# Performance work log

Measured on AMD Instinct MI355X. Metric: run time of the kernel, lower is better.

## Reference

```python
import jax, jax.numpy as jnp
import numpy as np

# Lloyd-Max (Max 1960) optimal 16-level quantizer for N(0,1), bits=4
_CODEBOOK_4 = np.array([-2.7326, -2.069, -1.6181, -1.2562, -0.9424, -0.6568,
                        -0.3881, -0.1284, 0.1284, 0.3881, 0.6568, 0.9424,
                        1.2562, 1.6181, 2.069, 2.7326], dtype=np.float32)
DIM = 256


def setup_inputs() -> dict:
    key = jax.random.key(0)
    kx, kq = jax.random.split(key)
    x = jax.random.normal(kx, (4, 4096, DIM), dtype=jnp.float32)
    # orthogonal rotation via QR of a Gaussian matrix (mirrors torch.linalg.qr)
    rotation, _ = jnp.linalg.qr(jax.random.normal(kq, (DIM, DIM), dtype=jnp.float32))
    codebook = jnp.asarray(_CODEBOOK_4)
    return {"x": x, "rotation": rotation, "codebook": codebook}


def reference(x, rotation, codebook):
    shape = x.shape
    d = shape[-1]
    sqrt_d = jnp.sqrt(jnp.asarray(d, dtype=x.dtype))
    x_flat = x.reshape(-1, d)                                   # (N, d)
    x_norm = jnp.maximum(
        jnp.linalg.norm(x_flat, axis=-1, keepdims=True), 1e-8)  # (N, 1)
    u = x_flat / x_norm                                         # unit vectors
    y_scaled = (u @ rotation.T) * sqrt_d                        # ~N(0,1) coords
    # nearest codebook entry per scalar coordinate: (N, d, K) -> argmin over K
    idx = jnp.argmin(jnp.abs(y_scaled[..., None] - codebook), axis=-1)
    y_hat = codebook[idx] / sqrt_d                              # (N, d)
    x_hat = (y_hat @ rotation) * x_norm                         # de-rotate, rescale
    return x_hat.reshape(shape)
```

## Files before the change

### kernel.cpp

```cpp
#include <hip/hip_runtime.h>

typedef _Float16 f16;
typedef _Float16 f16x4 __attribute__((ext_vector_type(4)));
typedef _Float16 f16x8 __attribute__((ext_vector_type(8)));
typedef float f32x16 __attribute__((ext_vector_type(16)));
typedef float f32x4 __attribute__((ext_vector_type(4)));

#define APITCH 264
#define WREG 67584

__global__ __launch_bounds__(1024) void prep_kernel(const float* __restrict__ R,
                                                    f16* __restrict__ ws) {
  __shared__ float Lrs[32][260];
  const int g = blockIdx.x;
  const int t = threadIdx.x;
  f16* W1h = ws;
  f16* W1l = ws + WREG;
  f16* W2h = ws + 2 * WREG;

  #pragma unroll
  for (int it = 0; it < 2; ++it) {
    int c = it * 1024 + t;
    int row = c >> 6, c4 = (c & 63) * 4;
    f32x4 v = *(const f32x4*)&R[(long)(32 * g + row) * 256 + c4];
    *(f32x4*)&Lrs[row][c4] = v;
  }
  __syncthreads();

  {
    int f_loc = t >> 6, l = t & 63;
    int k0 = 16 * f_loc + 8 * (l >> 5);
    const float* src = &Lrs[l & 31][k0];
    f16x8 h, lo;
    #pragma unroll
    for (int j = 0; j < 8; ++j) {
      float v = src[j] * 256.0f;
      f16 hh = (f16)v;
      h[j] = hh;
      lo[j] = (f16)(v - (float)hh);
    }
    long o = (long)(g * 16 + f_loc) * 512 + l * 8;
    *(f16x8*)(W1h + o) = h;
    *(f16x8*)(W1l + o) = lo;
  }

  {
    int gp = t >> 7, e = (t >> 6) & 1, l = t & 63;
    int lr0 = 16 * e + 8 * (l >> 5);
    int col = 32 * gp + (l & 31);
    f16x8 h;
    #pragma unroll
    for (int j = 0; j < 8; ++j) h[j] = (f16)Lrs[lr0 + j][col];
    long o = (long)(gp * 16 + 2 * g + e) * 512 + l * 8;
    *(f16x8*)(W2h + o) = h;
  }
}

__global__ __launch_bounds__(512, 4) void tq_main(
    const float* __restrict__ X, const float* __restrict__ CB,
    const f16* __restrict__ ws, float* __restrict__ OUT) {
  __shared__ f16 A1h[32][APITCH];
  __shared__ f16 A1l[32][APITCH];
  __shared__ float s2s[32];

  const int tid = threadIdx.x;
  const int lane = tid & 63;
  const int wv = tid >> 6;
  const int lrow = lane & 31;
  const int kg = lane >> 5;
  const long row0 = (long)blockIdx.x * 32;

  const f16* W1h = ws;
  const f16* W1l = ws + WREG;
  const f16* W2h = ws + 2 * WREG;

  const int r = tid >> 4, q = tid & 15;
  const float* xp = X + (row0 + r) * 256 + q * 16;
  float xa[16];
  #pragma unroll
  for (int i = 0; i < 4; ++i) {
    f32x4 v = ((const f32x4*)xp)[i];
    xa[4 * i] = v.x; xa[4 * i + 1] = v.y; xa[4 * i + 2] = v.z; xa[4 * i + 3] = v.w;
  }
  float ss = 0.f;
  #pragma unroll
  for (int i = 0; i < 16; ++i) ss += xa[i] * xa[i];
  ss += __shfl_xor(ss, 8, 16);
  ss += __shfl_xor(ss, 4, 16);
  ss += __shfl_xor(ss, 2, 16);
  ss += __shfl_xor(ss, 1, 16);
  float nrm = fmaxf(sqrtf(ss), 1e-8f);
  float s1f = 4096.0f / nrm;
  if (q == 0) s2s[r] = nrm * 0.0625f;

  #pragma unroll
  for (int c8 = 0; c8 < 2; ++c8) {
    f16x8 h, l;
    #pragma unroll
    for (int j = 0; j < 8; ++j) {
      float a = xa[c8 * 8 + j] * s1f;
      f16 hh = (f16)a;
      h[j] = hh;
      l[j] = (f16)(a - (float)hh);
    }
    *(f16x8*)&A1h[r][q * 16 + c8 * 8] = h;
    *(f16x8*)&A1l[r][q * 16 + c8 * 8] = l;
  }
  __syncthreads();

  const f16* W1hp = W1h + (long)(wv * 16) * 512 + lane * 8;
  const f16* W1lp = W1l + (long)(wv * 16) * 512 + lane * 8;
  f16x8 bh0 = *(const f16x8*)(W1hp);
  f16x8 bl0 = *(const f16x8*)(W1lp);
  f16x8 bh1 = *(const f16x8*)(W1hp + 512);
  f16x8 bl1 = *(const f16x8*)(W1lp + 512);

  f32x16 zv;
  #pragma unroll
  for (int i = 0; i < 16; ++i) zv[i] = 0.0f;
  f32x16 accH = zv, accL = zv;

  #pragma unroll
  for (int ks = 0; ks < 16; ks += 2) {
    {
      const int k0 = ks * 16 + kg * 8;
      f16x8 ah = *(const f16x8*)&A1h[lrow][k0];
      f16x8 al = *(const f16x8*)&A1l[lrow][k0];
      accH = __builtin_amdgcn_mfma_f32_32x32x16_f16(ah, bh0, accH, 0, 0, 0);
      accL = __builtin_amdgcn_mfma_f32_32x32x16_f16(al, bh0, accL, 0, 0, 0);
      accH = __builtin_amdgcn_mfma_f32_32x32x16_f16(ah, bl0, accH, 0, 0, 0);
      accL = __builtin_amdgcn_mfma_f32_32x32x16_f16(al, bl0, accL, 0, 0, 0);
      bh0 = *(const f16x8*)(W1hp + (ks + 2) * 512);
      bl0 = *(const f16x8*)(W1lp + (ks + 2) * 512);
    }
    {
      const int k0 = (ks + 1) * 16 + kg * 8;
      f16x8 ah = *(const f16x8*)&A1h[lrow][k0];
      f16x8 al = *(const f16x8*)&A1l[lrow][k0];
      accH = __builtin_amdgcn_mfma_f32_32x32x16_f16(ah, bh1, accH, 0, 0, 0);
      accL = __builtin_amdgcn_mfma_f32_32x32x16_f16(al, bh1, accL, 0, 0, 0);
      accH = __builtin_amdgcn_mfma_f32_32x32x16_f16(ah, bl1, accH, 0, 0, 0);
      accL = __builtin_amdgcn_mfma_f32_32x32x16_f16(al, bl1, accL, 0, 0, 0);
      bh1 = *(const f16x8*)(W1hp + (ks + 3) * 512);
      bl1 = *(const f16x8*)(W1lp + (ks + 3) * 512);
    }
  }
  f32x16 acc;
  #pragma unroll
  for (int i = 0; i < 16; ++i) acc[i] = accH[i] + accL[i];

  const f16* W2p = W2h + (long)(wv * 16) * 512 + lane * 8;
  f16x8 c0 = *(const f16x8*)(W2p);
  f16x8 c1 = *(const f16x8*)(W2p + 512);
  f16x8 c2 = *(const f16x8*)(W2p + 1024);
  f16x8 c3 = *(const f16x8*)(W2p + 1536);

  __syncthreads();

  float cbf[16];
  #pragma unroll
  for (int i = 0; i < 16; ++i) cbf[i] = CB[i];
  float M[15];
  #pragma unroll
  for (int t = 0; t < 15; ++t) M[t] = 65536.0f * (0.5f * (cbf[t] + cbf[t + 1]));
  unsigned int cpk[8];
  #pragma unroll
  for (int i = 0; i < 8; ++i) {
    unsigned short lb = __builtin_bit_cast(unsigned short, (f16)cbf[2 * i]);
    unsigned short hb = __builtin_bit_cast(unsigned short, (f16)cbf[2 * i + 1]);
    cpk[i] = ((unsigned int)hb << 16) | (unsigned int)lb;
  }

  f16 (*Qs)[APITCH] = A1h;
  #pragma unroll
  for (int rr = 0; rr < 16; ++rr) {
    float y = acc[rr];
    int row = 4 * kg + (rr & 3) + 8 * (rr >> 2);
    int kk = 32 * wv + lrow;
    bool b3 = y > M[7];
    float m2 = b3 ? M[11] : M[3];
    bool b2 = y > m2;
    float m1 = b3 ? (b2 ? M[13] : M[9]) : (b2 ? M[5] : M[1]);
    bool b1 = y > m1;
    float m0 = b1 ? (b3 ? (b2 ? M[14] : M[10]) : (b2 ? M[6] : M[2]))
                  : (b3 ? (b2 ? M[12] : M[8]) : (b2 ? M[4] : M[0]));
    bool b0 = y > m0;
    unsigned int pp = b3 ? (b2 ? (b1 ? cpk[7] : cpk[6]) : (b1 ? cpk[5] : cpk[4]))
                         : (b2 ? (b1 ? cpk[3] : cpk[2]) : (b1 ? cpk[1] : cpk[0]));
    unsigned short qb = (unsigned short)(b0 ? (pp >> 16) : (pp & 0xFFFFu));
    Qs[row][kk] = __builtin_bit_cast(f16, qb);
  }
  __syncthreads();

  f32x16 acc2a = zv, acc2b = zv;
  #pragma unroll
  for (int ks = 0; ks < 16; ks += 4) {
    {
      f16x8 qa = *(const f16x8*)&Qs[lrow][ks * 16 + kg * 8];
      acc2a = __builtin_amdgcn_mfma_f32_32x32x16_f16(qa, c0, acc2a, 0, 0, 0);
      c0 = *(const f16x8*)(W2p + (ks + 4) * 512);
    }
    {
      f16x8 qa = *(const f16x8*)&Qs[lrow][(ks + 1) * 16 + kg * 8];
      acc2b = __builtin_amdgcn_mfma_f32_32x32x16_f16(qa, c1, acc2b, 0, 0, 0);
      c1 = *(const f16x8*)(W2p + (ks + 5) * 512);
    }
    {
      f16x8 qa = *(const f16x8*)&Qs[lrow][(ks + 2) * 16 + kg * 8];
      acc2a = __builtin_amdgcn_mfma_f32_32x32x16_f16(qa, c2, acc2a, 0, 0, 0);
      c2 = *(const f16x8*)(W2p + (ks + 6) * 512);
    }
    {
      f16x8 qa = *(const f16x8*)&Qs[lrow][(ks + 3) * 16 + kg * 8];
      acc2b = __builtin_amdgcn_mfma_f32_32x32x16_f16(qa, c3, acc2b, 0, 0, 0);
      c3 = *(const f16x8*)(W2p + (ks + 7) * 512);
    }
  }

  #pragma unroll
  for (int rr = 0; rr < 16; ++rr) {
    int row = 4 * kg + (rr & 3) + 8 * (rr >> 2);
    int col = 32 * wv + lrow;
    OUT[(row0 + row) * 256 + col] = (acc2a[rr] + acc2b[rr]) * s2s[row];
  }
}

#define FB_APITCH 264
#define FB_B1PITCH 40
#define FB_B2PITCH 264

__global__ __launch_bounds__(256, 1) void tq_main_fb(
    const float* __restrict__ X, const float* __restrict__ R,
    const float* __restrict__ CB, float* __restrict__ OUT) {
  __shared__ f16 A1h[64][FB_APITCH];
  __shared__ f16 A1l[64][FB_APITCH];
  __shared__ f16 Qs[64][FB_APITCH];
  __shared__ f32x4 Braw[2624];
  __shared__ float pn[4][64];
  __shared__ float s1s[64];
  __shared__ float s2s[64];

  f16 (*B1h)[FB_B1PITCH] = (f16(*)[FB_B1PITCH])Braw;
  f16 (*B1l)[FB_B1PITCH] = (f16(*)[FB_B1PITCH])((char*)Braw + 20480);
  f16 (*B2h)[FB_B2PITCH] = (f16(*)[FB_B2PITCH])Braw;

  const int tid = threadIdx.x;
  const int lane = tid & 63;
  const int wv = tid >> 6;
  const int lrow = lane & 31;
  const int kg = lane >> 5;
  const long row0 = (long)blockIdx.x * 64;

  float cbf[16];
  #pragma unroll
  for (int i = 0; i < 16; ++i) cbf[i] = CB[i];
  float M[15];
  #pragma unroll
  for (int t = 0; t < 15; ++t) M[t] = 65536.0f * (0.5f * (cbf[t] + cbf[t + 1]));
  unsigned int cpk[8];
  #pragma unroll
  for (int i = 0; i < 8; ++i) {
    unsigned short lb = __builtin_bit_cast(unsigned short, (f16)cbf[2 * i]);
    unsigned short hb = __builtin_bit_cast(unsigned short, (f16)cbf[2 * i + 1]);
    cpk[i] = ((unsigned int)hb << 16) | (unsigned int)lb;
  }

  const int xrow = tid >> 2, xq = tid & 3;
  const float* xp = X + (row0 + xrow) * 256 + xq * 64;
  float xa[64];
  #pragma unroll
  for (int i = 0; i < 16; ++i) {
    f32x4 v = ((const f32x4*)xp)[i];
    xa[4 * i] = v.x; xa[4 * i + 1] = v.y; xa[4 * i + 2] = v.z; xa[4 * i + 3] = v.w;
  }
  float ss = 0.f;
  #pragma unroll
  for (int i = 0; i < 64; ++i) ss += xa[i] * xa[i];
  pn[xq][xrow] = ss;
  __syncthreads();
  if (tid < 64) {
    float s = pn[0][tid] + pn[1][tid] + pn[2][tid] + pn[3][tid];
    float nrm = fmaxf(sqrtf(s), 1e-8f);
    s1s[tid] = 4096.0f / nrm;
    s2s[tid] = nrm * 0.0625f;
  }
  __syncthreads();

  {
    float s1f = s1s[xrow];
    #pragma unroll
    for (int c8 = 0; c8 < 8; ++c8) {
      f16x8 h, l;
      #pragma unroll
      for (int j = 0; j < 8; ++j) {
        float a = xa[c8 * 8 + j] * s1f;
        f16 hh = (f16)a;
        h[j] = hh;
        l[j] = (f16)(a - (float)hh);
      }
      *(f16x8*)&A1h[xrow][xq * 64 + c8 * 8] = h;
      *(f16x8*)&A1l[xrow][xq * 64 + c8 * 8] = l;
    }
  }

  f32x4 pf[8];
  #pragma unroll
  for (int q = 0; q < 8; ++q) {
    int c = q * 256 + tid;
    pf[q] = *(const f32x4*)&R[(long)(c >> 3) * 256 + ((c & 7) * 4)];
  }

  f32x16 zv;
  #pragma unroll
  for (int i = 0; i < 16; ++i) zv[i] = 0.0f;
  f32x16 acc[2][2];
  acc[0][0] = zv; acc[0][1] = zv; acc[1][0] = zv; acc[1][1] = zv;

  for (int kp = 0; kp < 8; ++kp) {
    __syncthreads();
    #pragma unroll
    for (int q = 0; q < 8; ++q) {
      int c = q * 256 + tid;
      int n = c >> 3, k4 = (c & 7) * 4;
      f16x4 h, l;
      #pragma unroll
      for (int j = 0; j < 4; ++j) {
        float sv = pf[q][j] * 256.0f;
        f16 hh = (f16)sv;
        h[j] = hh;
        l[j] = (f16)(sv - (float)hh);
      }
      *(f16x4*)&B1h[n][k4] = h;
      *(f16x4*)&B1l[n][k4] = l;
    }
    __syncthreads();
    if (kp < 7) {
      #pragma unroll
      for (int q = 0; q < 8; ++q) {
        int c = q * 256 + tid;
        pf[q] = *(const f32x4*)&R[(long)(c >> 3) * 256 + (kp + 1) * 32 + ((c & 7) * 4)];
      }
    }
    #pragma unroll
    for (int ks = 0; ks < 2; ++ks) {
      const int k0 = kp * 32 + ks * 16 + kg * 8;
      const int lk = ks * 16 + kg * 8;
      f16x8 ah[2], al[2], bhf[2], blf[2];
      #pragma unroll
      for (int m = 0; m < 2; ++m) {
        ah[m] = *(const f16x8*)&A1h[32 * m + lrow][k0];
        al[m] = *(const f16x8*)&A1l[32 * m + lrow][k0];
      }
      #pragma unroll
      for (int n = 0; n < 2; ++n) {
        int col = 64 * wv + 32 * n + lrow;
        bhf[n] = *(const f16x8*)&B1h[col][lk];
        blf[n] = *(const f16x8*)&B1l[col][lk];
      }
      #pragma unroll
      for (int m = 0; m < 2; ++m)
        #pragma unroll
        for (int n = 0; n < 2; ++n) {
          acc[m][n] = __builtin_amdgcn_mfma_f32_32x32x16_f16(ah[m], bhf[n], acc[m][n], 0, 0, 0);
          acc[m][n] = __builtin_amdgcn_mfma_f32_32x32x16_f16(al[m], bhf[n], acc[m][n], 0, 0, 0);
          acc[m][n] = __builtin_amdgcn_mfma_f32_32x32x16_f16(ah[m], blf[n], acc[m][n], 0, 0, 0);
          acc[m][n] = __builtin_amdgcn_mfma_f32_32x32x16_f16(al[m], blf[n], acc[m][n], 0, 0, 0);
        }
    }
  }

  #pragma unroll
  for (int q = 0; q < 8; ++q) {
    int c = q * 256 + tid;
    pf[q] = *(const f32x4*)&R[(long)(c >> 6) * 256 + ((c & 63) * 4)];
  }

  #pragma unroll
  for (int m = 0; m < 2; ++m)
    #pragma unroll
    for (int n = 0; n < 2; ++n)
      #pragma unroll
      for (int rr = 0; rr < 16; ++rr) {
        float y = acc[m][n][rr];
        int row = 32 * m + 4 * kg + (rr & 3) + 8 * (rr >> 2);
        int kk = 64 * wv + 32 * n + lrow;
        bool b3 = y > M[7];
        float m2 = b3 ? M[11] : M[3];
        bool b2 = y > m2;
        float m1 = b3 ? (b2 ? M[13] : M[9]) : (b2 ? M[5] : M[1]);
        bool b1 = y > m1;
        float m0 = b1 ? (b3 ? (b2 ? M[14] : M[10]) : (b2 ? M[6] : M[2]))
                      : (b3 ? (b2 ? M[12] : M[8]) : (b2 ? M[4] : M[0]));
        bool b0 = y > m0;
        unsigned int pp = b3 ? (b2 ? (b1 ? cpk[7] : cpk[6]) : (b1 ? cpk[5] : cpk[4]))
                             : (b2 ? (b1 ? cpk[3] : cpk[2]) : (b1 ? cpk[1] : cpk[0]));
        unsigned short qb = (unsigned short)(b0 ? (pp >> 16) : (pp & 0xFFFFu));
        Qs[row][kk] = __builtin_bit_cast(f16, qb);
      }
  __syncthreads();

  f32x16 acc2[2][2];
  acc2[0][0] = zv; acc2[0][1] = zv; acc2[1][0] = zv; acc2[1][1] = zv;

  for (int kp = 0; kp < 8; ++kp) {
    if (kp) __syncthreads();
    #pragma unroll
    for (int q = 0; q < 8; ++q) {
      int c = q * 256 + tid;
      int k = c >> 6, n4 = (c & 63) * 4;
      f16x4 h;
      #pragma unroll
      for (int j = 0; j < 4; ++j) h[j] = (f16)pf[q][j];
      *(f16x4*)&B2h[k][n4] = h;
    }
    __syncthreads();
    if (kp < 7) {
      #pragma unroll
      for (int q = 0; q < 8; ++q) {
        int c = q * 256 + tid;
        pf[q] = *(const f32x4*)&R[(long)((kp + 1) * 32 + (c >> 6)) * 256 + ((c & 63) * 4)];
      }
    }
    #pragma unroll
    for (int ks = 0; ks < 2; ++ks) {
      const int k0 = kp * 32 + ks * 16 + kg * 8;
      const int lk = ks * 16 + kg * 8;
      f16x8 qa[2], bb[2];
      #pragma unroll
      for (int m = 0; m < 2; ++m) qa[m] = *(const f16x8*)&Qs[32 * m + lrow][k0];
      #pragma unroll
      for (int n = 0; n < 2; ++n) {
        int colg = 64 * wv + 32 * n + lrow;
        #pragma unroll
        for (int j = 0; j < 8; ++j) bb[n][j] = B2h[lk + j][colg];
      }
      #pragma unroll
      for (int m = 0; m < 2; ++m)
        #pragma unroll
        for (int n = 0; n < 2; ++n)
          acc2[m][n] = __builtin_amdgcn_mfma_f32_32x32x16_f16(qa[m], bb[n], acc2[m][n], 0, 0, 0);
    }
  }

  #pragma unroll
  for (int m = 0; m < 2; ++m)
    #pragma unroll
    for (int n = 0; n < 2; ++n)
      #pragma unroll
      for (int rr = 0; rr < 16; ++rr) {
        int row = 32 * m + 4 * kg + (rr & 3) + 8 * (rr >> 2);
        int col = 64 * wv + 32 * n + lrow;
        OUT[(row0 + row) * 256 + col] = acc2[m][n][rr] * s2s[row];
      }
}

extern "C" void kernel_launch(void* const* d_in, const int* in_sizes, int n_in,
                              void* d_out, int out_size, void* d_ws, size_t ws_size,
                              hipStream_t stream) {
  const float* X = (const float*)d_in[0];
  const float* R = (const float*)d_in[1];
  const float* CB = (const float*)d_in[2];
  float* OUT = (float*)d_out;
  const int nrows = in_sizes[0] / 256;

  if (ws_size >= (size_t)3 * WREG * sizeof(f16)) {
    f16* ws = (f16*)d_ws;
    prep_kernel<<<8, 1024, 0, stream>>>(R, ws);
    tq_main<<<nrows / 32, 512, 0, stream>>>(X, CB, ws, OUT);
  } else {
    tq_main_fb<<<nrows / 64, 256, 0, stream>>>(X, R, CB, OUT);
  }
}
```

Baseline: 27.13 us.

## Process 64 rows per block so each rotation fragment feeds two MFMA row tiles

The main kernel now handles 64 rows per block instead of 32, so every B fragment loaded from the prepared rotation workspace is reused across two 32-row MFMA tiles in both matmuls. This halves global weight traffic per row. The B-fragment prefetch depth grows from 2 to 4 stages, and the norm loads are issued before the reduction to overlap them. In exchange the block count halves (256 blocks), launch bounds drop to one block per SM hint, and register and LDS use per block grow, which may reduce occupancy and latency hiding.

New measurement: 31.36 us. +15.6%, slower.

```diff
diff --git a/kernel.cpp b/kernel.cpp
--- a/kernel.cpp
+++ b/kernel.cpp
@@ -56,57 +56,32 @@
   }
 }
 
-__global__ __launch_bounds__(512, 4) void tq_main(
+__global__ __launch_bounds__(512, 1) void tq_main(
     const float* __restrict__ X, const float* __restrict__ CB,
     const f16* __restrict__ ws, float* __restrict__ OUT) {
-  __shared__ f16 A1h[32][APITCH];
-  __shared__ f16 A1l[32][APITCH];
-  __shared__ float s2s[32];
+  __shared__ f16 A1h[64][APITCH];
+  __shared__ f16 A1l[64][APITCH];
+  __shared__ float s2s[64];
 
   const int tid = threadIdx.x;
   const int lane = tid & 63;
   const int wv = tid >> 6;
   const int lrow = lane & 31;
   const int kg = lane >> 5;
-  const long row0 = (long)blockIdx.x * 32;
+  const long row0 = (long)blockIdx.x * 64;
 
   const f16* W1h = ws;
   const f16* W1l = ws + WREG;
   const f16* W2h = ws + 2 * WREG;
 
-  const int r = tid >> 4, q = tid & 15;
-  const float* xp = X + (row0 + r) * 256 + q * 16;
-  float xa[16];
-  #pragma unroll
-  for (int i = 0; i < 4; ++i) {
+  const int r = tid >> 3, q = tid & 7;
+  const float* xp = X + (row0 + r) * 256 + q * 32;
+  float xa[32];
+  #pragma unroll
+  for (int i = 0; i < 8; ++i) {
     f32x4 v = ((const f32x4*)xp)[i];
     xa[4 * i] = v.x; xa[4 * i + 1] = v.y; xa[4 * i + 2] = v.z; xa[4 * i + 3] = v.w;
   }
-  float ss = 0.f;
-  #pragma unroll
-  for (int i = 0; i < 16; ++i) ss += xa[i] * xa[i];
-  ss += __shfl_xor(ss, 8, 16);
-  ss += __shfl_xor(ss, 4, 16);
-  ss += __shfl_xor(ss, 2, 16);
-  ss += __shfl_xor(ss, 1, 16);
-  float nrm = fmaxf(sqrtf(ss), 1e-8f);
-  float s1f = 4096.0f / nrm;
-  if (q == 0) s2s[r] = nrm * 0.0625f;
-
-  #pragma unroll
-  for (int c8 = 0; c8 < 2; ++c8) {
-    f16x8 h, l;
-    #pragma unroll
-    for (int j = 0; j < 8; ++j) {
-      float a = xa[c8 * 8 + j] * s1f;
-      f16 hh = (f16)a;
-      h[j] = hh;
-      l[j] = (f16)(a - (float)hh);
-    }
-    *(f16x8*)&A1h[r][q * 16 + c8 * 8] = h;
-    *(f16x8*)&A1l[r][q * 16 + c8 * 8] = l;
-  }
-  __syncthreads();
 
   const f16* W1hp = W1h + (long)(wv * 16) * 512 + lane * 8;
   const f16* W1lp = W1l + (long)(wv * 16) * 512 + lane * 8;
@@ -114,40 +89,72 @@
   f16x8 bl0 = *(const f16x8*)(W1lp);
   f16x8 bh1 = *(const f16x8*)(W1hp + 512);
   f16x8 bl1 = *(const f16x8*)(W1lp + 512);
+  f16x8 bh2 = *(const f16x8*)(W1hp + 1024);
+  f16x8 bl2 = *(const f16x8*)(W1lp + 1024);
+  f16x8 bh3 = *(const f16x8*)(W1hp + 1536);
+  f16x8 bl3 = *(const f16x8*)(W1lp + 1536);
+
+  float ss = 0.f;
+  #pragma unroll
+  for (int i = 0; i < 32; ++i) ss += xa[i] * xa[i];
+  ss += __shfl_xor(ss, 4, 8);
+  ss += __shfl_xor(ss, 2, 8);
+  ss += __shfl_xor(ss, 1, 8);
+  float nrm = fmaxf(sqrtf(ss), 1e-8f);
+  float s1f = 4096.0f / nrm;
+  if (q == 0) s2s[r] = nrm * 0.0625f;
+
+  #pragma unroll
+  for (int c8 = 0; c8 < 4; ++c8) {
+    f16x8 h, l;
+    #pragma unroll
+    for (int j = 0; j < 8; ++j) {
+      float a = xa[c8 * 8 + j] * s1f;
+      f16 hh = (f16)a;
+      h[j] = hh;
+      l[j] = (f16)(a - (float)hh);
+    }
+    *(f16x8*)&A1h[r][q * 32 + c8 * 8] = h;
+    *(f16x8*)&A1l[r][q * 32 + c8 * 8] = l;
+  }
+  __syncthreads();
 
   f32x16 zv;
   #pragma unroll
   for (int i = 0; i < 16; ++i) zv[i] = 0.0f;
-  f32x16 accH = zv, accL = zv;
-
-  #pragma unroll
-  for (int ks = 0; ks < 16; ks += 2) {
-    {
-      const int k0 = ks * 16 + kg * 8;
-      f16x8 ah = *(const f16x8*)&A1h[lrow][k0];
-      f16x8 al = *(const f16x8*)&A1l[lrow][k0];
-      accH = __builtin_amdgcn_mfma_f32_32x32x16_f16(ah, bh0, accH, 0, 0, 0);
-      accL = __builtin_amdgcn_mfma_f32_32x32x16_f16(al, bh0, accL, 0, 0, 0);
-      accH = __builtin_amdgcn_mfma_f32_32x32x16_f16(ah, bl0, accH, 0, 0, 0);
-      accL = __builtin_amdgcn_mfma_f32_32x32x16_f16(al, bl0, accL, 0, 0, 0);
-      bh0 = *(const f16x8*)(W1hp + (ks + 2) * 512);
-      bl0 = *(const f16x8*)(W1lp + (ks + 2) * 512);
-    }
-    {
-      const int k0 = (ks + 1) * 16 + kg * 8;
-      f16x8 ah = *(const f16x8*)&A1h[lrow][k0];
-      f16x8 al = *(const f16x8*)&A1l[lrow][k0];
-      accH = __builtin_amdgcn_mfma_f32_32x32x16_f16(ah, bh1, accH, 0, 0, 0);
-      accL = __builtin_amdgcn_mfma_f32_32x32x16_f16(al, bh1, accL, 0, 0, 0);
-      accH = __builtin_amdgcn_mfma_f32_32x32x16_f16(ah, bl1, accH, 0, 0, 0);
-      accL = __builtin_amdgcn_mfma_f32_32x32x16_f16(al, bl1, accL, 0, 0, 0);
-      bh1 = *(const f16x8*)(W1hp + (ks + 3) * 512);
-      bl1 = *(const f16x8*)(W1lp + (ks + 3) * 512);
-    }
-  }
-  f32x16 acc;
-  #pragma unroll
-  for (int i = 0; i < 16; ++i) acc[i] = accH[i] + accL[i];
+  f32x16 accH0 = zv, accL0 = zv, accH1 = zv, accL1 = zv;
+
+#define MM1_STAGE(BH, BL, KS)                                                   \
+  {                                                                             \
+    const int k0 = (KS) * 16 + kg * 8;                                          \
+    f16x8 ah0 = *(const f16x8*)&A1h[lrow][k0];                                  \
+    f16x8 al0 = *(const f16x8*)&A1l[lrow][k0];                                  \
+    f16x8 ah1 = *(const f16x8*)&A1h[32 + lrow][k0];                             \
+    f16x8 al1 = *(const f16x8*)&A1l[32 + lrow][k0];                             \
+    accH0 = __builtin_amdgcn_mfma_f32_32x32x16_f16(ah0, BH, accH0, 0, 0, 0);    \
+    accL0 = __builtin_amdgcn_mfma_f32_32x32x16_f16(al0, BH, accL0, 0, 0, 0);    \
+    accH1 = __builtin_amdgcn_mfma_f32_32x32x16_f16(ah1, BH, accH1, 0, 0, 0);    \
+    accL1 = __builtin_amdgcn_mfma_f32_32x32x16_f16(al1, BH, accL1, 0, 0, 0);    \
+    accH0 = __builtin_amdgcn_mfma_f32_32x32x16_f16(ah0, BL, accH0, 0, 0, 0);    \
+    accL0 = __builtin_amdgcn_mfma_f32_32x32x16_f16(al0, BL, accL0, 0, 0, 0);    \
+    accH1 = __builtin_amdgcn_mfma_f32_32x32x16_f16(ah1, BL, accH1, 0, 0, 0);    \
+    accL1 = __builtin_amdgcn_mfma_f32_32x32x16_f16(al1, BL, accL1, 0, 0, 0);    \
+    BH = *(const f16x8*)(W1hp + ((KS) + 4) * 512);                              \
+    BL = *(const f16x8*)(W1lp + ((KS) + 4) * 512);                              \
+  }
+
+  #pragma unroll
+  for (int ksb = 0; ksb < 16; ksb += 4) {
+    MM1_STAGE(bh0, bl0, ksb)
+    MM1_STAGE(bh1, bl1, ksb + 1)
+    MM1_STAGE(bh2, bl2, ksb + 2)
+    MM1_STAGE(bh3, bl3, ksb + 3)
+  }
+#undef MM1_STAGE
+
+  f32x16 acc0, acc1;
+  #pragma unroll
+  for (int i = 0; i < 16; ++i) { acc0[i] = accH0[i] + accL0[i]; acc1[i] = accH1[i] + accL1[i]; }
 
   const f16* W2p = W2h + (long)(wv * 16) * 512 + lane * 8;
   f16x8 c0 = *(const f16x8*)(W2p);
@@ -173,55 +180,59 @@
 
   f16 (*Qs)[APITCH] = A1h;
   #pragma unroll
-  for (int rr = 0; rr < 16; ++rr) {
-    float y = acc[rr];
-    int row = 4 * kg + (rr & 3) + 8 * (rr >> 2);
-    int kk = 32 * wv + lrow;
-    bool b3 = y > M[7];
-    float m2 = b3 ? M[11] : M[3];
-    bool b2 = y > m2;
-    float m1 = b3 ? (b2 ? M[13] : M[9]) : (b2 ? M[5] : M[1]);
-    bool b1 = y > m1;
-    float m0 = b1 ? (b3 ? (b2 ? M[14] : M[10]) : (b2 ? M[6] : M[2]))
-                  : (b3 ? (b2 ? M[12] : M[8]) : (b2 ? M[4] : M[0]));
-    bool b0 = y > m0;
-    unsigned int pp = b3 ? (b2 ? (b1 ? cpk[7] : cpk[6]) : (b1 ? cpk[5] : cpk[4]))
-                         : (b2 ? (b1 ? cpk[3] : cpk[2]) : (b1 ? cpk[1] : cpk[0]));
-    unsigned short qb = (unsigned short)(b0 ? (pp >> 16) : (pp & 0xFFFFu));
-    Qs[row][kk] = __builtin_bit_cast(f16, qb);
-  }
-  __syncthreads();
-
-  f32x16 acc2a = zv, acc2b = zv;
-  #pragma unroll
-  for (int ks = 0; ks < 16; ks += 4) {
-    {
-      f16x8 qa = *(const f16x8*)&Qs[lrow][ks * 16 + kg * 8];
-      acc2a = __builtin_amdgcn_mfma_f32_32x32x16_f16(qa, c0, acc2a, 0, 0, 0);
-      c0 = *(const f16x8*)(W2p + (ks + 4) * 512);
-    }
-    {
-      f16x8 qa = *(const f16x8*)&Qs[lrow][(ks + 1) * 16 + kg * 8];
-      acc2b = __builtin_amdgcn_mfma_f32_32x32x16_f16(qa, c1, acc2b, 0, 0, 0);
-      c1 = *(const f16x8*)(W2p + (ks + 5) * 512);
-    }
-    {
-      f16x8 qa = *(const f16x8*)&Qs[lrow][(ks + 2) * 16 + kg * 8];
-      acc2a = __builtin_amdgcn_mfma_f32_32x32x16_f16(qa, c2, acc2a, 0, 0, 0);
-      c2 = *(const f16x8*)(W2p + (ks + 6) * 512);
-    }
-    {
-      f16x8 qa = *(const f16x8*)&Qs[lrow][(ks + 3) * 16 + kg * 8];
-      acc2b = __builtin_amdgcn_mfma_f32_32x32x16_f16(qa, c3, acc2b, 0, 0, 0);
-      c3 = *(const f16x8*)(W2p + (ks + 7) * 512);
-    }
-  }
-
-  #pragma unroll
-  for (int rr = 0; rr < 16; ++rr) {
-    int row = 4 * kg + (rr & 3) + 8 * (rr >> 2);
-    int col = 32 * wv + lrow;
-    OUT[(row0 + row) * 256 + col] = (acc2a[rr] + acc2b[rr]) * s2s[row];
+  for (int m = 0; m < 2; ++m) {
+    const f32x16& am = m ? acc1 : acc0;
+    #pragma unroll
+    for (int rr = 0; rr < 16; ++rr) {
+      float y = am[rr];
+      int row = 32 * m + 4 * kg + (rr & 3) + 8 * (rr >> 2);
+      int kk = 32 * wv + lrow;
+      bool b3 = y > M[7];
+      float m2 = b3 ? M[11] : M[3];
+      bool b2 = y > m2;
+      float m1 = b3 ? (b2 ? M[13] : M[9]) : (b2 ? M[5] : M[1]);
+      bool b1 = y > m1;
+      float m0 = b1 ? (b3 ? (b2 ? M[14] : M[10]) : (b2 ? M[6] : M[2]))
+                    : (b3 ? (b2 ? M[12] : M[8]) : (b2 ? M[4] : M[0]));
+      bool b0 = y > m0;
+      unsigned int pp = b3 ? (b2 ? (b1 ? cpk[7] : cpk[6]) : (b1 ? cpk[5] : cpk[4]))
+                           : (b2 ? (b1 ? cpk[3] : cpk[2]) : (b1 ? cpk[1] : cpk[0]));
+      unsigned short qb = (unsigned short)(b0 ? (pp >> 16) : (pp & 0xFFFFu));
+      Qs[row][kk] = __builtin_bit_cast(f16, qb);
+    }
+  }
+  __syncthreads();
+
+  f32x16 acc2_0 = zv, acc2_1 = zv;
+
+#define MM2_STAGE(CS, KS)                                                       \
+  {                                                                             \
+    const int k0 = (KS) * 16 + kg * 8;                                          \
+    f16x8 qa0 = *(const f16x8*)&Qs[lrow][k0];                                   \
+    f16x8 qa1 = *(const f16x8*)&Qs[32 + lrow][k0];                              \
+    acc2_0 = __builtin_amdgcn_mfma_f32_32x32x16_f16(qa0, CS, acc2_0, 0, 0, 0);  \
+    acc2_1 = __builtin_amdgcn_mfma_f32_32x32x16_f16(qa1, CS, acc2_1, 0, 0, 0);  \
+    CS = *(const f16x8*)(W2p + ((KS) + 4) * 512);                               \
+  }
+
+  #pragma unroll
+  for (int ksb = 0; ksb < 16; ksb += 4) {
+    MM2_STAGE(c0, ksb)
+    MM2_STAGE(c1, ksb + 1)
+    MM2_STAGE(c2, ksb + 2)
+    MM2_STAGE(c3, ksb + 3)
+  }
+#undef MM2_STAGE
+
+  #pragma unroll
+  for (int m = 0; m < 2; ++m) {
+    const f32x16& am = m ? acc2_1 : acc2_0;
+    #pragma unroll
+    for (int rr = 0; rr < 16; ++rr) {
+      int row = 32 * m + 4 * kg + (rr & 3) + 8 * (rr >> 2);
+      int col = 32 * wv + lrow;
+      OUT[(row0 + row) * 256 + col] = am[rr] * s2s[row];
+    }
   }
 }
 
@@ -466,7 +477,7 @@
   if (ws_size >= (size_t)3 * WREG * sizeof(f16)) {
     f16* ws = (f16*)d_ws;
     prep_kernel<<<8, 1024, 0, stream>>>(R, ws);
-    tq_main<<<nrows / 32, 512, 0, stream>>>(X, CB, ws, OUT);
+    tq_main<<<nrows / 64, 512, 0, stream>>>(X, CB, ws, OUT);
   } else {
     tq_main_fb<<<nrows / 64, 256, 0, stream>>>(X, R, CB, OUT);
   }
```

## Split prep kernel across more blocks, drop lo*lo MFMA terms, hoist codebook load

Applied to the files above, without the earlier changes.

The prep kernel now runs on 32 blocks of 512 threads instead of 8 blocks of 1024. Each block handles a quarter of a group's split-weight outputs, so the tiny setup kernel is spread over more CUs. In the main kernel, the low-times-low split-precision MFMA products in the first GEMM are removed, cutting a quarter of the first-stage matrix ops at a small accuracy cost. The codebook load moves early to hide latency, and the barrier sits after the threshold setup. The accumulators are summed inline during quantization.

Measured after the change: 26.12 us. 1.04x faster.

```diff
diff --git a/kernel.cpp b/kernel.cpp
--- a/kernel.cpp
+++ b/kernel.cpp
@@ -9,50 +9,50 @@
 #define APITCH 264
 #define WREG 67584
 
-__global__ __launch_bounds__(1024) void prep_kernel(const float* __restrict__ R,
-                                                    f16* __restrict__ ws) {
+__global__ __launch_bounds__(512) void prep_kernel(const float* __restrict__ R,
+                                                   f16* __restrict__ ws) {
   __shared__ float Lrs[32][260];
-  const int g = blockIdx.x;
+  const int b = blockIdx.x;
+  const int g = b >> 2, h = b & 3;
   const int t = threadIdx.x;
   f16* W1h = ws;
   f16* W1l = ws + WREG;
   f16* W2h = ws + 2 * WREG;
 
   #pragma unroll
-  for (int it = 0; it < 2; ++it) {
-    int c = it * 1024 + t;
+  for (int it = 0; it < 4; ++it) {
+    int c = it * 512 + t;
     int row = c >> 6, c4 = (c & 63) * 4;
     f32x4 v = *(const f32x4*)&R[(long)(32 * g + row) * 256 + c4];
     *(f32x4*)&Lrs[row][c4] = v;
   }
   __syncthreads();
 
-  {
-    int f_loc = t >> 6, l = t & 63;
+  if (t < 256) {
+    int f_loc = 4 * h + (t >> 6), l = t & 63;
     int k0 = 16 * f_loc + 8 * (l >> 5);
     const float* src = &Lrs[l & 31][k0];
-    f16x8 h, lo;
+    f16x8 hi, lo;
     #pragma unroll
     for (int j = 0; j < 8; ++j) {
       float v = src[j] * 256.0f;
       f16 hh = (f16)v;
-      h[j] = hh;
+      hi[j] = hh;
       lo[j] = (f16)(v - (float)hh);
     }
     long o = (long)(g * 16 + f_loc) * 512 + l * 8;
-    *(f16x8*)(W1h + o) = h;
+    *(f16x8*)(W1h + o) = hi;
     *(f16x8*)(W1l + o) = lo;
-  }
-
-  {
-    int gp = t >> 7, e = (t >> 6) & 1, l = t & 63;
+  } else {
+    int u = t - 256;
+    int gp = 2 * h + (u >> 7), e = (u >> 6) & 1, l = u & 63;
     int lr0 = 16 * e + 8 * (l >> 5);
     int col = 32 * gp + (l & 31);
-    f16x8 h;
-    #pragma unroll
-    for (int j = 0; j < 8; ++j) h[j] = (f16)Lrs[lr0 + j][col];
+    f16x8 hv;
+    #pragma unroll
+    for (int j = 0; j < 8; ++j) hv[j] = (f16)Lrs[lr0 + j][col];
     long o = (long)(gp * 16 + 2 * g + e) * 512 + l * 8;
-    *(f16x8*)(W2h + o) = h;
+    *(f16x8*)(W2h + o) = hv;
   }
 }
 
@@ -82,6 +82,11 @@
     f32x4 v = ((const f32x4*)xp)[i];
     xa[4 * i] = v.x; xa[4 * i + 1] = v.y; xa[4 * i + 2] = v.z; xa[4 * i + 3] = v.w;
   }
+
+  float cbf[16];
+  #pragma unroll
+  for (int i = 0; i < 16; ++i) cbf[i] = CB[i];
+
   float ss = 0.f;
   #pragma unroll
   for (int i = 0; i < 16; ++i) ss += xa[i] * xa[i];
@@ -129,7 +134,6 @@
       accH = __builtin_amdgcn_mfma_f32_32x32x16_f16(ah, bh0, accH, 0, 0, 0);
       accL = __builtin_amdgcn_mfma_f32_32x32x16_f16(al, bh0, accL, 0, 0, 0);
       accH = __builtin_amdgcn_mfma_f32_32x32x16_f16(ah, bl0, accH, 0, 0, 0);
-      accL = __builtin_amdgcn_mfma_f32_32x32x16_f16(al, bl0, accL, 0, 0, 0);
       bh0 = *(const f16x8*)(W1hp + (ks + 2) * 512);
       bl0 = *(const f16x8*)(W1lp + (ks + 2) * 512);
     }
@@ -140,14 +144,10 @@
       accH = __builtin_amdgcn_mfma_f32_32x32x16_f16(ah, bh1, accH, 0, 0, 0);
       accL = __builtin_amdgcn_mfma_f32_32x32x16_f16(al, bh1, accL, 0, 0, 0);
       accH = __builtin_amdgcn_mfma_f32_32x32x16_f16(ah, bl1, accH, 0, 0, 0);
-      accL = __builtin_amdgcn_mfma_f32_32x32x16_f16(al, bl1, accL, 0, 0, 0);
       bh1 = *(const f16x8*)(W1hp + (ks + 3) * 512);
       bl1 = *(const f16x8*)(W1lp + (ks + 3) * 512);
     }
   }
-  f32x16 acc;
-  #pragma unroll
-  for (int i = 0; i < 16; ++i) acc[i] = accH[i] + accL[i];
 
   const f16* W2p = W2h + (long)(wv * 16) * 512 + lane * 8;
   f16x8 c0 = *(const f16x8*)(W2p);
@@ -155,11 +155,6 @@
   f16x8 c2 = *(const f16x8*)(W2p + 1024);
   f16x8 c3 = *(const f16x8*)(W2p + 1536);
 
-  __syncthreads();
-
-  float cbf[16];
-  #pragma unroll
-  for (int i = 0; i < 16; ++i) cbf[i] = CB[i];
   float M[15];
   #pragma unroll
   for (int t = 0; t < 15; ++t) M[t] = 65536.0f * (0.5f * (cbf[t] + cbf[t + 1]));
@@ -171,10 +166,12 @@
     cpk[i] = ((unsigned int)hb << 16) | (unsigned int)lb;
   }
 
+  __syncthreads();
+
   f16 (*Qs)[APITCH] = A1h;
   #pragma unroll
   for (int rr = 0; rr < 16; ++rr) {
-    float y = acc[rr];
+    float y = accH[rr] + accL[rr];
     int row = 4 * kg + (rr & 3) + 8 * (rr >> 2);
     int kk = 32 * wv + lrow;
     bool b3 = y > M[7];
@@ -465,7 +462,7 @@
 
   if (ws_size >= (size_t)3 * WREG * sizeof(f16)) {
     f16* ws = (f16*)d_ws;
-    prep_kernel<<<8, 1024, 0, stream>>>(R, ws);
+    prep_kernel<<<32, 512, 0, stream>>>(R, ws);
     tq_main<<<nrows / 32, 512, 0, stream>>>(X, CB, ws, OUT);
   } else {
     tq_main_fb<<<nrows / 64, 256, 0, stream>>>(X, R, CB, OUT);
```
